# Kernel tuning notes

Hardware: AMD Instinct MI355X
Metric: run time of the kernel (lower is better)

The kernel has to match this reference:

```python
import jax, jax.numpy as jnp
import numpy as np

N, D, L, H = 4, 512, 2048, 8  # batch, feat_dim, seq_len, num_heads


def setup_inputs() -> dict:
    key = jax.random.key(0)
    k1, k2, k3, k4 = jax.random.split(key, 4)
    x = jax.random.normal(k1, (N, D, L), dtype=jnp.float32)
    w_qkv = jax.random.normal(k2, (3 * D, D, 1), dtype=jnp.float32) * 0.02   # 1x1 conv
    w_dw = jax.random.normal(k3, (3 * D, 1, 3), dtype=jnp.float32) * 0.02    # depthwise k=3
    w_proj = jax.random.normal(k4, (D, D, 1), dtype=jnp.float32) * 0.02      # 1x1 conv
    temperature = jnp.ones((1, H, 1, 1), dtype=jnp.float32)
    return {"x": x, "w_qkv": w_qkv, "w_dw": w_dw, "w_proj": w_proj, "temperature": temperature}


def _conv1x1(x, w):
    # x: (n, c_in, l), w: (c_out, c_in, 1)
    return jnp.einsum('oc,ncl->nol', w[:, :, 0], x)


def _l2norm(t, eps=1e-12):
    # matches F.normalize: t / max(||t||_2, eps) along last dim
    n = jnp.sqrt(jnp.sum(t * t, axis=-1, keepdims=True))
    return t / jnp.maximum(n, eps)


def reference(x, w_qkv, w_dw, w_proj, temperature):
    n, d, l = x.shape
    h = temperature.shape[1]
    dh = d // h

    qkv = _conv1x1(x, w_qkv)                               # (n, 3d, l)
    qkv = jax.lax.conv_general_dilated(
        qkv, w_dw, window_strides=(1,), padding=[(1, 1)],
        dimension_numbers=('NCH', 'OIH', 'NCH'),
        feature_group_count=3 * d)                          # depthwise conv, (n, 3d, l)

    q, k, v = jnp.split(qkv, 3, axis=1)                     # each (n, d, l)
    # (n, d, l) -> (n, h, dh, l) -> (n, h, l, dh)
    q = q.reshape(n, h, dh, l).transpose(0, 1, 3, 2)
    k = k.reshape(n, h, dh, l).transpose(0, 1, 3, 2)
    v = v.reshape(n, h, dh, l).transpose(0, 1, 3, 2)

    q = _l2norm(q)
    k = _l2norm(k)

    scores = jnp.einsum('nhqd,nhkd->nhqk', q, k) * temperature  # (n, h, l, l)
    attn = jax.nn.softmax(scores, axis=-1)
    out = jnp.einsum('nhqk,nhkd->nhqd', attn, v)                # (n, h, l, dh)
    out = out.transpose(0, 1, 3, 2).reshape(n, d, l)            # (n, d, l)
    return _conv1x1(out, w_proj)
```

## Files before the change

### kernel.cpp

```cpp
#include <hip/hip_runtime.h>
#include <hip/hip_bf16.h>
#include <cstdint>
#include <cstddef>

#define N_B 4
#define D_F 512
#define L_S 2048
#define H_N 8
#define DH  64
#define C3  (3*D_F)

typedef __attribute__((ext_vector_type(8)))  short short8;
typedef __attribute__((ext_vector_type(4)))  float f32x4;
typedef __attribute__((ext_vector_type(16))) float f32x16;

__device__ __forceinline__ unsigned int pk_bf16(float a, float b) {
    __hip_bfloat162 h = __float22bfloat162_rn(float2{a, b});
    union { __hip_bfloat162 h; unsigned int u; } cv;
    cv.h = h;
    return cv.u;
}
__device__ __forceinline__ unsigned short bf16_rn(float f) {
    union { float f; unsigned int u; } c; c.f = f;
    unsigned int r = c.u + 0x7FFF + ((c.u >> 16) & 1);
    return (unsigned short)(r >> 16);
}
__device__ __forceinline__ float bf16_f(unsigned short h) {
    union { unsigned int u; float f; } c; c.u = ((unsigned int)h) << 16;
    return c.f;
}

__device__ __forceinline__ void gll16(const unsigned short* g, unsigned short* l) {
    __builtin_amdgcn_global_load_lds(
        (const __attribute__((address_space(1))) unsigned int*)g,
        (__attribute__((address_space(3))) unsigned int*)l,
        16, 0, 0);
}

__global__ __launch_bounds__(256) void cvt_split(const float* __restrict__ src,
                                                 unsigned short* __restrict__ hi,
                                                 unsigned short* __restrict__ lo,
                                                 int n4) {
    int i = blockIdx.x * 256 + threadIdx.x;
    if (i >= n4) return;
    float4 v = ((const float4*)src)[i];
    ushort4 h, l;
    h.x = bf16_rn(v.x); l.x = bf16_rn(v.x - bf16_f(h.x));
    h.y = bf16_rn(v.y); l.y = bf16_rn(v.y - bf16_f(h.y));
    h.z = bf16_rn(v.z); l.z = bf16_rn(v.z - bf16_f(h.z));
    h.w = bf16_rn(v.w); l.w = bf16_rn(v.w - bf16_f(h.w));
    ((ushort4*)hi)[i] = h;
    ((ushort4*)lo)[i] = l;
}

__global__ __launch_bounds__(256) void cvt_xT(const float* __restrict__ x,
                                              unsigned short* __restrict__ xT,
                                              int C) {
    __shared__ float tile[64][65];
    const int tid = threadIdx.x;
    const int l0  = blockIdx.x * 64;
    const int c0  = blockIdx.y * 64;
    const int n   = blockIdx.z;

    const float* xn = x + (size_t)n * C * L_S;
#pragma unroll
    for (int r = 0; r < 16; ++r) {
        int c = r * 4 + (tid >> 6);
        int l = tid & 63;
        tile[c][l] = xn[(size_t)(c0 + c) * L_S + l0 + l];
    }
    __syncthreads();

    unsigned short* xn_t = xT + (size_t)n * L_S * C;
#pragma unroll
    for (int r = 0; r < 8; ++r) {
        int l  = r * 8 + (tid >> 5);
        int cp = tid & 31;
        unsigned int pk = pk_bf16(tile[cp * 2][l], tile[cp * 2 + 1][l]);
        *(unsigned int*)&xn_t[(size_t)(l0 + l) * C + c0 + cp * 2] = pk;
    }
}

template<int SPLIT, int OUT_BF16>
__global__ __launch_bounds__(256) void gemm_mfma2(const unsigned short* __restrict__ Whi,
                                                  const unsigned short* __restrict__ Wlo,
                                                  const unsigned short* __restrict__ XThi,
                                                  const unsigned short* __restrict__ XTlo,
                                                  void* __restrict__ Y,
                                                  int O, int C) {
    __shared__ unsigned short Wt[SPLIT ? 2 : 1][4][128 * 8];
    __shared__ unsigned short Xt[SPLIT ? 2 : 1][4][128 * 8];

    const int tid  = threadIdx.x;
    const int lane = tid & 63;
    const int w    = tid >> 6;
    const int g    = lane >> 4;
    const int c    = lane & 15;
    const int wr   = (w >> 1) * 64;
    const int wc   = (w & 1) * 64;
    const int l0   = blockIdx.x * 128;
    const int o0   = blockIdx.y * 128;
    const int n    = blockIdx.z;

    const unsigned short* XTn_hi = XThi + (size_t)n * L_S * C;
    const unsigned short* XTn_lo = SPLIT ? (XTlo + (size_t)n * L_S * C) : nullptr;

    const int rhalf = (w & 1) * 64;
    const int cpA   = w >> 1;
    const int cpB   = 2 + (w >> 1);
    const size_t wrowA = (size_t)(o0 + rhalf + lane) * C;
    const size_t xrowA = (size_t)(l0 + rhalf + lane) * C;

    f32x4 acc[4][4];
#pragma unroll
    for (int mt = 0; mt < 4; ++mt)
#pragma unroll
        for (int nt = 0; nt < 4; ++nt) acc[mt][nt] = (f32x4){0.f, 0.f, 0.f, 0.f};

    for (int c0 = 0; c0 < C; c0 += 32) {
        __syncthreads();
        gll16(Whi + wrowA + c0 + cpA * 8, &Wt[0][cpA][rhalf * 8]);
        gll16(Whi + wrowA + c0 + cpB * 8, &Wt[0][cpB][rhalf * 8]);
        gll16(XTn_hi + xrowA + c0 + cpA * 8, &Xt[0][cpA][rhalf * 8]);
        gll16(XTn_hi + xrowA + c0 + cpB * 8, &Xt[0][cpB][rhalf * 8]);
        if (SPLIT) {
            gll16(Wlo + wrowA + c0 + cpA * 8, &Wt[1][cpA][rhalf * 8]);
            gll16(Wlo + wrowA + c0 + cpB * 8, &Wt[1][cpB][rhalf * 8]);
            gll16(XTn_lo + xrowA + c0 + cpA * 8, &Xt[1][cpA][rhalf * 8]);
            gll16(XTn_lo + xrowA + c0 + cpB * 8, &Xt[1][cpB][rhalf * 8]);
        }
        __syncthreads();

        short8 a0[4], b0[4];
#pragma unroll
        for (int mt = 0; mt < 4; ++mt) a0[mt] = *(short8*)&Wt[0][g][(wr + mt * 16 + c) * 8];
#pragma unroll
        for (int nt = 0; nt < 4; ++nt) b0[nt] = *(short8*)&Xt[0][g][(wc + nt * 16 + c) * 8];

        if (SPLIT) {
            short8 a1[4], b1[4];
#pragma unroll
            for (int mt = 0; mt < 4; ++mt) a1[mt] = *(short8*)&Wt[1][g][(wr + mt * 16 + c) * 8];
#pragma unroll
            for (int nt = 0; nt < 4; ++nt) b1[nt] = *(short8*)&Xt[1][g][(wc + nt * 16 + c) * 8];
#pragma unroll
            for (int mt = 0; mt < 4; ++mt)
#pragma unroll
                for (int nt = 0; nt < 4; ++nt) {
                    acc[mt][nt] = __builtin_amdgcn_mfma_f32_16x16x32_bf16(a0[mt], b0[nt], acc[mt][nt], 0, 0, 0);
                    acc[mt][nt] = __builtin_amdgcn_mfma_f32_16x16x32_bf16(a0[mt], b1[nt], acc[mt][nt], 0, 0, 0);
                    acc[mt][nt] = __builtin_amdgcn_mfma_f32_16x16x32_bf16(a1[mt], b0[nt], acc[mt][nt], 0, 0, 0);
                }
        } else {
#pragma unroll
            for (int mt = 0; mt < 4; ++mt)
#pragma unroll
                for (int nt = 0; nt < 4; ++nt)
                    acc[mt][nt] = __builtin_amdgcn_mfma_f32_16x16x32_bf16(a0[mt], b0[nt], acc[mt][nt], 0, 0, 0);
        }
    }

#pragma unroll
    for (int mt = 0; mt < 4; ++mt) {
#pragma unroll
        for (int r = 0; r < 4; ++r) {
            int oo = o0 + wr + mt * 16 + g * 4 + r;
            size_t rowbase = ((size_t)n * O + oo) * L_S;
#pragma unroll
            for (int nt = 0; nt < 4; ++nt) {
                int ll = l0 + wc + nt * 16 + c;
                if (OUT_BF16)
                    ((unsigned short*)Y)[rowbase + ll] = bf16_rn(acc[mt][nt][r]);
                else
                    ((float*)Y)[rowbase + ll] = acc[mt][nt][r];
            }
        }
    }
}

__global__ __launch_bounds__(256) void fused_qk2(const unsigned short* __restrict__ qkv_bf,
                                                 const float* __restrict__ w_dw,
                                                 unsigned short* __restrict__ Qb,
                                                 unsigned short* __restrict__ Kb) {
    __shared__ unsigned short rows[64 * 264];
    __shared__ float wsm[192];
    const int tid = threadIdx.x;
    const int l0  = blockIdx.x * 256;
    const int gg  = blockIdx.y;
    const int n   = blockIdx.z;
    const int head = gg & 7;
    const int ch0  = (gg < 8) ? head * 64 : 512 + head * 64;

    if (tid < 192) wsm[tid] = w_dw[ch0 * 3 + tid];

    const unsigned short* base = qkv_bf + ((size_t)n * C3 + ch0) * L_S;
    for (int f = tid; f < 2048; f += 256) {
        int e = f >> 5, s = f & 31;
        *(uint4*)&rows[e * 264 + s * 8] = *(const uint4*)&base[(size_t)e * L_S + l0 + s * 8];
    }
    if (tid < 64) {
        rows[tid * 264 + 256] = (l0 > 0) ? base[(size_t)tid * L_S + l0 - 1] : (unsigned short)0;
    } else if (tid < 128) {
        int e = tid - 64;
        rows[e * 264 + 257] = (l0 + 256 < L_S) ? base[(size_t)e * L_S + l0 + 256] : (unsigned short)0;
    }
    __syncthreads();

    const int lL = tid;
    const int iL = (lL == 0)   ? 256 : lL - 1;
    const int iR = (lL == 255) ? 257 : lL + 1;
    float y[64];
    float s = 0.f;
#pragma unroll
    for (int e = 0; e < 64; ++e) {
        float a = bf16_f(rows[e * 264 + iL]);
        float b = bf16_f(rows[e * 264 + lL]);
        float d = bf16_f(rows[e * 264 + iR]);
        float v = wsm[e * 3 + 0] * a + wsm[e * 3 + 1] * b + wsm[e * 3 + 2] * d;
        y[e] = v;
        s += v * v;
    }
    float sc = 1.0f / fmaxf(sqrtf(s), 1e-12f);

    const int l = l0 + tid;
    unsigned short* dst = ((gg < 8) ? Qb : Kb) + (size_t)(n * H_N + head) * 8 * L_S * 8;
#pragma unroll
    for (int p = 0; p < 8; ++p) {
        uint4 pk = make_uint4(pk_bf16(y[8 * p + 0] * sc, y[8 * p + 1] * sc),
                              pk_bf16(y[8 * p + 2] * sc, y[8 * p + 3] * sc),
                              pk_bf16(y[8 * p + 4] * sc, y[8 * p + 5] * sc),
                              pk_bf16(y[8 * p + 6] * sc, y[8 * p + 7] * sc));
        *(uint4*)&dst[((size_t)p * L_S + l) * 8] = pk;
    }
}

__global__ __launch_bounds__(256) void fused_v2(const unsigned short* __restrict__ qkv_bf,
                                                const float* __restrict__ w_dw,
                                                unsigned short* __restrict__ Vb) {
    const int tid = threadIdx.x;
    const int e   = tid & 63;
    const int jp  = blockIdx.x * 4 + (tid >> 6);
    const int h   = blockIdx.y;
    const int n   = blockIdx.z;
    const int ch  = 1024 + h * 64 + e;
    const unsigned short* row = qkv_bf + ((size_t)n * C3 + ch) * L_S;
    const int k0 = jp * 8;

    uint4 mv = *(const uint4*)&row[k0];
    unsigned int lw = (jp > 0)   ? *(const unsigned int*)&row[k0 - 2] : 0u;
    unsigned int rw = (jp < 255) ? *(const unsigned int*)&row[k0 + 8] : 0u;

    float v[10];
    v[0] = bf16_f((unsigned short)(lw >> 16));
    v[1] = bf16_f((unsigned short)(mv.x & 0xFFFF));
    v[2] = bf16_f((unsigned short)(mv.x >> 16));
    v[3] = bf16_f((unsigned short)(mv.y & 0xFFFF));
    v[4] = bf16_f((unsigned short)(mv.y >> 16));
    v[5] = bf16_f((unsigned short)(mv.z & 0xFFFF));
    v[6] = bf16_f((unsigned short)(mv.z >> 16));
    v[7] = bf16_f((unsigned short)(mv.w & 0xFFFF));
    v[8] = bf16_f((unsigned short)(mv.w >> 16));
    v[9] = bf16_f((unsigned short)(rw & 0xFFFF));

    float w0 = w_dw[ch * 3 + 0], w1 = w_dw[ch * 3 + 1], w2 = w_dw[ch * 3 + 2];
    unsigned int o[4];
#pragma unroll
    for (int i = 0; i < 4; ++i) {
        float y0 = w0 * v[2 * i + 0] + w1 * v[2 * i + 1] + w2 * v[2 * i + 2];
        float y1 = w0 * v[2 * i + 1] + w1 * v[2 * i + 2] + w2 * v[2 * i + 3];
        o[i] = pk_bf16(y0, y1);
    }
    uint4 ov = make_uint4(o[0], o[1], o[2], o[3]);
    *(uint4*)&Vb[(((size_t)(n * H_N + h) * 256 + jp) * 512) + e * 8] = ov;
}

__global__ __launch_bounds__(512, 4) void attn7(const unsigned short* __restrict__ Qb,
                                                const unsigned short* __restrict__ Kb,
                                                const unsigned short* __restrict__ Vb,
                                                const float* __restrict__ temp,
                                                unsigned short* __restrict__ aoT_hi,
                                                unsigned short* __restrict__ aoT_lo) {
    __shared__ unsigned short KV[32768];
    __shared__ float smA[128], smB[128];
    float* OtB = (float*)(KV + 16384);
    float* OtA = (float*)KV;

    const int tid  = threadIdx.x;
    const int lane = tid & 63;
    const int w    = tid >> 6;
    const int g2   = w >> 2;
    const int wv   = w & 3;
    const int c32  = lane & 31;
    const int h    = lane >> 5;
    const int q0   = blockIdx.x * 128;
    const int hd   = blockIdx.y;
    const int n    = blockIdx.z;

    const size_t hb = (size_t)(n * H_N + hd);
    const unsigned short* Qh = Qb + hb * 8 * L_S * 8;
    const unsigned short* Kh = Kb + hb * 8 * L_S * 8;
    const unsigned short* Vh = Vb + hb * 256 * 512;
    const float t    = temp[hd];
    const float negm = -fabsf(t);

    unsigned short* myKV = KV + g2 * 16384;
    unsigned short* Qs   = KV + 24576;

    for (int tk = w; tk < 48; tk += 8) {
        if (tk < 16) {
            int p = tk >> 1, hh = tk & 1;
            gll16(Qh + ((size_t)p * L_S + q0 + hh * 64 + lane) * 8, Qs + p * 1024 + hh * 512);
        } else if (tk < 24) {
            int p = tk - 16;
            gll16(Kh + ((size_t)p * L_S + lane) * 8, KV + p * 512);
        } else if (tk < 32) {
            int p = tk - 24;
            gll16(Vh + ((size_t)p * 512 + lane * 8), KV + 4096 + p * 512);
        } else if (tk < 40) {
            int p = tk - 32;
            gll16(Kh + ((size_t)p * L_S + 64 + lane) * 8, KV + 16384 + p * 512);
        } else {
            int p = tk - 40;
            gll16(Vh + ((size_t)(8 + p) * 512 + lane * 8), KV + 16384 + 4096 + p * 512);
        }
    }
    __syncthreads();

    short8 qa[4];
#pragma unroll
    for (int es = 0; es < 4; ++es)
        qa[es] = *(short8*)&Qs[(es * 2 + h) * 1024 + (wv * 32 + c32) * 8];
    __syncthreads();

    f32x16 acc0, acc1;
#pragma unroll
    for (int i = 0; i < 16; ++i) { acc0[i] = 0.f; acc1[i] = 0.f; }
    float sumP = 0.f;

    for (int it = 0; it < 16; ++it) {
        const int cur = it & 1;
        const unsigned short* B = myKV + cur * 8192;

        if (it < 15) {
            const int kb = ((it + 1) * 2 + g2) * 64;
            unsigned short* D = myKV + (cur ^ 1) * 8192;
            gll16(Kh + ((size_t)wv * L_S + kb + lane) * 8,            D + wv * 512);
            gll16(Kh + ((size_t)(wv + 4) * L_S + kb + lane) * 8,      D + (wv + 4) * 512);
            gll16(Vh + ((size_t)(kb / 8 + wv) * 512 + lane * 8),      D + 4096 + wv * 512);
            gll16(Vh + ((size_t)(kb / 8 + wv + 4) * 512 + lane * 8),  D + 4096 + (wv + 4) * 512);
        }

        f32x16 sf0, sf1;
#pragma unroll
        for (int i = 0; i < 16; ++i) { sf0[i] = 0.f; sf1[i] = 0.f; }
#pragma unroll
        for (int es = 0; es < 4; ++es) {
            short8 ka0 = *(short8*)&B[(es * 2 + h) * 512 + c32 * 8];
            short8 ka1 = *(short8*)&B[(es * 2 + h) * 512 + (32 + c32) * 8];
            sf0 = __builtin_amdgcn_mfma_f32_32x32x16_bf16(ka0, qa[es], sf0, 0, 0, 0);
            sf1 = __builtin_amdgcn_mfma_f32_32x32x16_bf16(ka1, qa[es], sf1, 0, 0, 0);
        }

        short8 pa[4];
        {
            unsigned int W_[16], R_[16];
#pragma unroll
            for (int G = 0; G < 4; ++G) {
                float p0 = __expf(fmaf(sf0[4*G+0], t, negm));
                float p1 = __expf(fmaf(sf0[4*G+1], t, negm));
                float p2 = __expf(fmaf(sf0[4*G+2], t, negm));
                float p3 = __expf(fmaf(sf0[4*G+3], t, negm));
                sumP += (p0 + p1) + (p2 + p3);
                W_[2*G]   = pk_bf16(p0, p1);
                W_[2*G+1] = pk_bf16(p2, p3);
                float u0 = __expf(fmaf(sf1[4*G+0], t, negm));
                float u1 = __expf(fmaf(sf1[4*G+1], t, negm));
                float u2 = __expf(fmaf(sf1[4*G+2], t, negm));
                float u3 = __expf(fmaf(sf1[4*G+3], t, negm));
                sumP += (u0 + u1) + (u2 + u3);
                W_[8+2*G]   = pk_bf16(u0, u1);
                W_[8+2*G+1] = pk_bf16(u2, u3);
            }
#pragma unroll
            for (int j = 0; j < 16; ++j) R_[j] = __shfl_xor(W_[j], 32);
#pragma unroll
            for (int ks = 0; ks < 4; ++ks) {
                const int bb = (ks >> 1) * 8;
                const int m4 = (ks & 1) * 4;
                unsigned int a0 = h ? R_[bb+m4+2] : W_[bb+m4+0];
                unsigned int a1 = h ? R_[bb+m4+3] : W_[bb+m4+1];
                unsigned int a2 = h ? W_[bb+m4+2] : R_[bb+m4+0];
                unsigned int a3 = h ? W_[bb+m4+3] : R_[bb+m4+1];
                uint4 pu = make_uint4(a0, a1, a2, a3);
                pa[ks] = *(short8*)&pu;
            }
        }

#pragma unroll
        for (int ks = 0; ks < 4; ++ks) {
            short8 vb0 = *(short8*)&B[4096 + (ks * 2 + h) * 512 + c32 * 8];
            short8 vb1 = *(short8*)&B[4096 + (ks * 2 + h) * 512 + (32 + c32) * 8];
            acc0 = __builtin_amdgcn_mfma_f32_32x32x16_bf16(pa[ks], vb0, acc0, 0, 0, 0);
            acc1 = __builtin_amdgcn_mfma_f32_32x32x16_bf16(pa[ks], vb1, acc1, 0, 0, 0);
        }

        __syncthreads();
    }

    sumP += __shfl_xor(sumP, 32);

    if (g2 == 1) {
        smB[wv * 32 + c32] = sumP;
#pragma unroll
        for (int r = 0; r < 16; ++r) {
            int ql = (r & 3) + 8 * (r >> 2) + 4 * h;
            int qg = wv * 32 + ql;
            OtB[qg * 64 + c32]      = acc0[r];
            OtB[qg * 64 + 32 + c32] = acc1[r];
        }
    } else {
        smA[wv * 32 + c32] = sumP;
    }
    __syncthreads();

    if (g2 == 0) {
#pragma unroll
        for (int r = 0; r < 16; ++r) {
            int ql = (r & 3) + 8 * (r >> 2) + 4 * h;
            int qg = wv * 32 + ql;
            float inv = 1.0f / (smA[qg] + smB[qg]);
            float v0 = (acc0[r] + OtB[qg * 64 + c32])      * inv;
            float v1 = (acc1[r] + OtB[qg * 64 + 32 + c32]) * inv;
            OtA[qg * 64 + (c32 ^ (qg & 31))]        = v0;
            OtA[qg * 64 + ((32 + c32) ^ (qg & 31))] = v1;
        }
    }
    __syncthreads();

    for (int tt = tid; tt < 8192; tt += 512) {
        int qq = tt >> 6, e = tt & 63;
        float v = OtA[qq * 64 + (e ^ (qq & 31))];
        unsigned short hi_ = bf16_rn(v);
        unsigned short lo_ = bf16_rn(v - bf16_f(hi_));
        size_t off = ((size_t)n * L_S + q0 + qq) * D_F + hd * 64 + e;
        aoT_hi[off] = hi_;
        aoT_lo[off] = lo_;
    }
}

extern "C" void kernel_launch(void* const* d_in, const int* in_sizes, int n_in,
                              void* d_out, int out_size, void* d_ws, size_t ws_size,
                              hipStream_t stream) {
    const float* x      = (const float*)d_in[0];
    const float* w_qkv  = (const float*)d_in[1];
    const float* w_dw   = (const float*)d_in[2];
    const float* w_proj = (const float*)d_in[3];
    const float* temp   = (const float*)d_in[4];
    float* out = (float*)d_out;

    const size_t WQE = (size_t)C3 * D_F;
    const size_t WPE = (size_t)D_F * D_F;

    char* ws = (char*)d_ws;
    unsigned short* qkv_bf = (unsigned short*)ws;
    unsigned short* Qb     = (unsigned short*)(ws + 25165824);
    unsigned short* Kb     = (unsigned short*)(ws + 33554432);
    unsigned short* Vb     = (unsigned short*)(ws + 41943040);
    unsigned short* xT     = (unsigned short*)(ws + 50331648);
    unsigned short* aoT_lo = (unsigned short*)(ws + 58720256);
    unsigned short* wq_hi  = (unsigned short*)(ws + 67108864);
    unsigned short* wq_lo  = wq_hi + WQE;
    unsigned short* wp_hi  = (unsigned short*)(ws + 70254592);
    unsigned short* wp_lo  = wp_hi + WPE;
    unsigned short* aoT_hi = xT;

    cvt_xT<<<dim3(L_S / 64, D_F / 64, N_B), 256, 0, stream>>>(x, xT, D_F);
    cvt_split<<<dim3((WQE / 4 + 255) / 256), 256, 0, stream>>>(w_qkv, wq_hi, wq_lo, WQE / 4);
    cvt_split<<<dim3((WPE / 4 + 255) / 256), 256, 0, stream>>>(w_proj, wp_hi, wp_lo, WPE / 4);

    gemm_mfma2<0, 1><<<dim3(L_S / 128, C3 / 128, N_B), 256, 0, stream>>>(
        wq_hi, nullptr, xT, nullptr, qkv_bf, C3, D_F);

    fused_qk2<<<dim3(L_S / 256, 16, N_B), 256, 0, stream>>>(qkv_bf, w_dw, Qb, Kb);
    fused_v2<<<dim3(64, H_N, N_B), 256, 0, stream>>>(qkv_bf, w_dw, Vb);

    attn7<<<dim3(L_S / 128, H_N, N_B), 512, 0, stream>>>(Qb, Kb, Vb, temp, aoT_hi, aoT_lo);

    gemm_mfma2<1, 0><<<dim3(L_S / 128, D_F / 128, N_B), 256, 0, stream>>>(
        wp_hi, wp_lo, aoT_hi, aoT_lo, out, D_F, D_F);
}
```

Baseline: 152.2 us.

## Load K/V directly from global into registers in attention, drop LDS staging

Rewrites the attention kernel to use 256-thread blocks where each wave reads Q, K and V straight from global memory (relying on L2/L1 reuse) instead of double-buffered LDS staging with a split-K across two wave groups. This removes the per-iteration block barriers, the LDS traffic and the cross-group partial-sum merge, and adds s_setprio around the MFMA sections. The risk is higher global/L2 load latency without explicit prefetch overlap, more registers for the preloaded fragments, and half as many waves per block.

New measurement: 154.2 us. No clear change (+1.3%).

```diff
diff --git a/kernel.cpp b/kernel.cpp
--- a/kernel.cpp
+++ b/kernel.cpp
@@ -274,22 +274,18 @@
     *(uint4*)&Vb[(((size_t)(n * H_N + h) * 256 + jp) * 512) + e * 8] = ov;
 }
 
-__global__ __launch_bounds__(512, 4) void attn7(const unsigned short* __restrict__ Qb,
+__global__ __launch_bounds__(256, 3) void attn8(const unsigned short* __restrict__ Qb,
                                                 const unsigned short* __restrict__ Kb,
                                                 const unsigned short* __restrict__ Vb,
                                                 const float* __restrict__ temp,
                                                 unsigned short* __restrict__ aoT_hi,
                                                 unsigned short* __restrict__ aoT_lo) {
-    __shared__ unsigned short KV[32768];
-    __shared__ float smA[128], smB[128];
-    float* OtB = (float*)(KV + 16384);
-    float* OtA = (float*)KV;
+    __shared__ float Ot[128 * 64];
+    __shared__ float sm[128];
 
     const int tid  = threadIdx.x;
     const int lane = tid & 63;
     const int w    = tid >> 6;
-    const int g2   = w >> 2;
-    const int wv   = w & 3;
     const int c32  = lane & 31;
     const int h    = lane >> 5;
     const int q0   = blockIdx.x * 128;
@@ -303,63 +299,42 @@
     const float t    = temp[hd];
     const float negm = -fabsf(t);
 
-    unsigned short* myKV = KV + g2 * 16384;
-    unsigned short* Qs   = KV + 24576;
-
-    for (int tk = w; tk < 48; tk += 8) {
-        if (tk < 16) {
-            int p = tk >> 1, hh = tk & 1;
-            gll16(Qh + ((size_t)p * L_S + q0 + hh * 64 + lane) * 8, Qs + p * 1024 + hh * 512);
-        } else if (tk < 24) {
-            int p = tk - 16;
-            gll16(Kh + ((size_t)p * L_S + lane) * 8, KV + p * 512);
-        } else if (tk < 32) {
-            int p = tk - 24;
-            gll16(Vh + ((size_t)p * 512 + lane * 8), KV + 4096 + p * 512);
-        } else if (tk < 40) {
-            int p = tk - 32;
-            gll16(Kh + ((size_t)p * L_S + 64 + lane) * 8, KV + 16384 + p * 512);
-        } else {
-            int p = tk - 40;
-            gll16(Vh + ((size_t)(8 + p) * 512 + lane * 8), KV + 16384 + 4096 + p * 512);
-        }
-    }
-    __syncthreads();
-
     short8 qa[4];
 #pragma unroll
     for (int es = 0; es < 4; ++es)
-        qa[es] = *(short8*)&Qs[(es * 2 + h) * 1024 + (wv * 32 + c32) * 8];
-    __syncthreads();
+        qa[es] = *(const short8*)&Qh[((size_t)(es * 2 + h) * L_S + q0 + w * 32 + c32) * 8];
 
     f32x16 acc0, acc1;
 #pragma unroll
     for (int i = 0; i < 16; ++i) { acc0[i] = 0.f; acc1[i] = 0.f; }
     float sumP = 0.f;
 
-    for (int it = 0; it < 16; ++it) {
-        const int cur = it & 1;
-        const unsigned short* B = myKV + cur * 8192;
-
-        if (it < 15) {
-            const int kb = ((it + 1) * 2 + g2) * 64;
-            unsigned short* D = myKV + (cur ^ 1) * 8192;
-            gll16(Kh + ((size_t)wv * L_S + kb + lane) * 8,            D + wv * 512);
-            gll16(Kh + ((size_t)(wv + 4) * L_S + kb + lane) * 8,      D + (wv + 4) * 512);
-            gll16(Vh + ((size_t)(kb / 8 + wv) * 512 + lane * 8),      D + 4096 + wv * 512);
-            gll16(Vh + ((size_t)(kb / 8 + wv + 4) * 512 + lane * 8),  D + 4096 + (wv + 4) * 512);
+    for (int k0 = 0; k0 < L_S; k0 += 64) {
+        short8 vb0[4], vb1[4];
+#pragma unroll
+        for (int ks = 0; ks < 4; ++ks) {
+            const unsigned short* vrow = Vh + (size_t)((k0 >> 3) + ks * 2 + h) * 512;
+            vb0[ks] = *(const short8*)&vrow[c32 * 8];
+            vb1[ks] = *(const short8*)&vrow[(32 + c32) * 8];
         }
 
         f32x16 sf0, sf1;
 #pragma unroll
         for (int i = 0; i < 16; ++i) { sf0[i] = 0.f; sf1[i] = 0.f; }
+        short8 ka0[4], ka1[4];
 #pragma unroll
         for (int es = 0; es < 4; ++es) {
-            short8 ka0 = *(short8*)&B[(es * 2 + h) * 512 + c32 * 8];
-            short8 ka1 = *(short8*)&B[(es * 2 + h) * 512 + (32 + c32) * 8];
-            sf0 = __builtin_amdgcn_mfma_f32_32x32x16_bf16(ka0, qa[es], sf0, 0, 0, 0);
-            sf1 = __builtin_amdgcn_mfma_f32_32x32x16_bf16(ka1, qa[es], sf1, 0, 0, 0);
-        }
+            const unsigned short* krow = Kh + (size_t)(es * 2 + h) * L_S * 8;
+            ka0[es] = *(const short8*)&krow[(k0 + c32) * 8];
+            ka1[es] = *(const short8*)&krow[(k0 + 32 + c32) * 8];
+        }
+        __builtin_amdgcn_s_setprio(1);
+#pragma unroll
+        for (int es = 0; es < 4; ++es) {
+            sf0 = __builtin_amdgcn_mfma_f32_32x32x16_bf16(ka0[es], qa[es], sf0, 0, 0, 0);
+            sf1 = __builtin_amdgcn_mfma_f32_32x32x16_bf16(ka1[es], qa[es], sf1, 0, 0, 0);
+        }
+        __builtin_amdgcn_s_setprio(0);
 
         short8 pa[4];
         {
@@ -396,50 +371,37 @@
             }
         }
 
+        __builtin_amdgcn_s_setprio(1);
 #pragma unroll
         for (int ks = 0; ks < 4; ++ks) {
-            short8 vb0 = *(short8*)&B[4096 + (ks * 2 + h) * 512 + c32 * 8];
-            short8 vb1 = *(short8*)&B[4096 + (ks * 2 + h) * 512 + (32 + c32) * 8];
-            acc0 = __builtin_amdgcn_mfma_f32_32x32x16_bf16(pa[ks], vb0, acc0, 0, 0, 0);
-            acc1 = __builtin_amdgcn_mfma_f32_32x32x16_bf16(pa[ks], vb1, acc1, 0, 0, 0);
-        }
-
-        __syncthreads();
+            acc0 = __builtin_amdgcn_mfma_f32_32x32x16_bf16(pa[ks], vb0[ks], acc0, 0, 0, 0);
+            acc1 = __builtin_amdgcn_mfma_f32_32x32x16_bf16(pa[ks], vb1[ks], acc1, 0, 0, 0);
+        }
+        __builtin_amdgcn_s_setprio(0);
     }
 
     sumP += __shfl_xor(sumP, 32);
-
-    if (g2 == 1) {
-        smB[wv * 32 + c32] = sumP;
-#pragma unroll
-        for (int r = 0; r < 16; ++r) {
-            int ql = (r & 3) + 8 * (r >> 2) + 4 * h;
-            int qg = wv * 32 + ql;
-            OtB[qg * 64 + c32]      = acc0[r];
-            OtB[qg * 64 + 32 + c32] = acc1[r];
-        }
-    } else {
-        smA[wv * 32 + c32] = sumP;
+    sm[w * 32 + c32] = 1.0f / sumP;
+
+    float inv[16];
+#pragma unroll
+    for (int r = 0; r < 16; ++r) {
+        int ql = (r & 3) + 8 * (r >> 2) + 4 * h;
+        inv[r] = sm[w * 32 + ql];
+    }
+
+#pragma unroll
+    for (int r = 0; r < 16; ++r) {
+        int ql = (r & 3) + 8 * (r >> 2) + 4 * h;
+        int qg = w * 32 + ql;
+        Ot[qg * 64 + (c32 ^ (qg & 31))]        = acc0[r] * inv[r];
+        Ot[qg * 64 + ((32 + c32) ^ (qg & 31))] = acc1[r] * inv[r];
     }
     __syncthreads();
 
-    if (g2 == 0) {
-#pragma unroll
-        for (int r = 0; r < 16; ++r) {
-            int ql = (r & 3) + 8 * (r >> 2) + 4 * h;
-            int qg = wv * 32 + ql;
-            float inv = 1.0f / (smA[qg] + smB[qg]);
-            float v0 = (acc0[r] + OtB[qg * 64 + c32])      * inv;
-            float v1 = (acc1[r] + OtB[qg * 64 + 32 + c32]) * inv;
-            OtA[qg * 64 + (c32 ^ (qg & 31))]        = v0;
-            OtA[qg * 64 + ((32 + c32) ^ (qg & 31))] = v1;
-        }
-    }
-    __syncthreads();
-
-    for (int tt = tid; tt < 8192; tt += 512) {
+    for (int tt = tid; tt < 8192; tt += 256) {
         int qq = tt >> 6, e = tt & 63;
-        float v = OtA[qq * 64 + (e ^ (qq & 31))];
+        float v = Ot[qq * 64 + (e ^ (qq & 31))];
         unsigned short hi_ = bf16_rn(v);
         unsigned short lo_ = bf16_rn(v - bf16_f(hi_));
         size_t off = ((size_t)n * L_S + q0 + qq) * D_F + hd * 64 + e;
@@ -484,7 +446,7 @@
     fused_qk2<<<dim3(L_S / 256, 16, N_B), 256, 0, stream>>>(qkv_bf, w_dw, Qb, Kb);
     fused_v2<<<dim3(64, H_N, N_B), 256, 0, stream>>>(qkv_bf, w_dw, Vb);
 
-    attn7<<<dim3(L_S / 128, H_N, N_B), 512, 0, stream>>>(Qb, Kb, Vb, temp, aoT_hi, aoT_lo);
+    attn8<<<dim3(L_S / 128, H_N, N_B), 256, 0, stream>>>(Qb, Kb, Vb, temp, aoT_hi, aoT_lo);
 
     gemm_mfma2<1, 0><<<dim3(L_S / 128, D_F / 128, N_B), 256, 0, stream>>>(
         wp_hi, wp_lo, aoT_hi, aoT_lo, out, D_F, D_F);
```
